# Performance work log

Measured on AMD Instinct MI355X. Metric: run time of the kernel, lower is better.

The kernel has to match this reference:

```python
import jax, jax.numpy as jnp
import numpy as np

B, S, D = 4, 2048, 1024
NEG_INF = jnp.float32(-jnp.inf)


def setup_inputs() -> dict:
    key = jax.random.key(0)
    kx, kq, kk, kv = jax.random.split(key, 4)
    scale = 0.02
    return {
        "x": jax.random.normal(kx, (B, S, D), dtype=jnp.float32),
        "Wq": jax.random.normal(kq, (D, D), dtype=jnp.float32) * scale,
        "Wk": jax.random.normal(kk, (D, D), dtype=jnp.float32) * scale,
        "Wv": jax.random.normal(kv, (D, D), dtype=jnp.float32) * scale,
    }


def reference(x, Wq, Wk, Wv):
    # nn.Linear(d_in, d_out): y = x @ W.T (no bias; qkv_bias=False)
    q = jnp.einsum("bsd,ed->bse", x, Wq)
    k = jnp.einsum("bsd,ed->bse", x, Wk)
    v = jnp.einsum("bsd,ed->bse", x, Wv)
    n = x.shape[1]
    scores = jnp.einsum("bqe,bke->bqk", q, k)  # [B, S, S]
    # causal mask: positions k > q are masked with -inf
    causal = jnp.tril(jnp.ones((n, n), dtype=bool))
    scores = jnp.where(causal[None, :, :], scores, NEG_INF)
    attn = jax.nn.softmax(scores / jnp.sqrt(jnp.float32(k.shape[-1])), axis=-1)
    # dropout p=0.0 (eval) -> identity
    return jnp.einsum("bqk,bke->bqe", attn, v)
```

## Files before the change

### kernel.cpp

```cpp
#include <hip/hip_runtime.h>
#include <hip/hip_bf16.h>
#include <stdint.h>
#include <stddef.h>


typedef __hip_bfloat16 bf16;
typedef short short8 __attribute__((ext_vector_type(8)));
typedef short short4v __attribute__((ext_vector_type(4)));
typedef float f32x4 __attribute__((ext_vector_type(4)));

#define BM 256
#define BN 128
#define BK 64
#define MSZ 8192
#define DD 1024

__device__ __forceinline__ void cstore(float* p, float v) { *p = v; }
__device__ __forceinline__ void cstore(bf16* p, float v) { *p = __float2bfloat16(v); }

__global__ __launch_bounds__(256)
void f2b(const float* __restrict__ s, bf16* __restrict__ d, int n) {
  const int i = (blockIdx.x * 256 + threadIdx.x) * 4;
  if (i >= n) return;
  const float4 v = *(const float4*)(s + i);
  bf16 t[4] = {__float2bfloat16(v.x), __float2bfloat16(v.y),
               __float2bfloat16(v.z), __float2bfloat16(v.w)};
  *(short4v*)(d + i) = *(short4v*)t;
}

__global__ __launch_bounds__(256)
void f2b3(const float* __restrict__ a, const float* __restrict__ b,
          const float* __restrict__ c, bf16* __restrict__ d, int n) {
  const float* s = (blockIdx.y == 0) ? a : (blockIdx.y == 1) ? b : c;
  const int i = (blockIdx.x * 256 + threadIdx.x) * 4;
  if (i >= n) return;
  const float4 v = *(const float4*)(s + i);
  bf16 t[4] = {__float2bfloat16(v.x), __float2bfloat16(v.y),
               __float2bfloat16(v.z), __float2bfloat16(v.w)};
  *(short4v*)(d + (size_t)blockIdx.y * n + i) = *(short4v*)t;
}

template <int MODE, typename CT>
__global__ __launch_bounds__(512, 4)
void gemm_bt(const bf16* __restrict__ A, const bf16* __restrict__ B,
             CT* __restrict__ C, bf16* __restrict__ C2,
             int lda, int ldb, int ldc, int K,
             long sA, long sB, long sC, float scale) {
  int by, bx;
  if (MODE == 2) {
    const int t = blockIdx.x;
    by = (int)((__fsqrt_rn(4.f * (float)t + 1.f) - 1.f) * 0.5f);
    while ((by + 1) * (by + 2) <= t) by++;
    while (by * (by + 1) > t) by--;
    bx = t - by * (by + 1);
  } else if (MODE == 3) {
    by = gridDim.y - 1 - blockIdx.y;
    bx = blockIdx.x;
  } else {
    by = blockIdx.y;
    bx = blockIdx.x;
  }

  __shared__ short8 As[2048];
  __shared__ short8 Bs[1024];

  const int tid = threadIdx.x;
  const int wave = tid >> 6, lane = tid & 63;
  const int wm = wave >> 1, wn = wave & 1;
  const int l15 = lane & 15, q4 = lane >> 4;
  const int bm0 = by * BM, bn0 = bx * BN;

  const bf16* Az = A + (long)blockIdx.z * sA;
  const bf16* Bz = B + (long)blockIdx.z * sB;
  CT* Cz = C + (long)blockIdx.z * sC;

  const int sg = lane >> 3, sr = lane & 7;
  const bf16* apg = Az + (size_t)(bm0 + wave * 32 + sr) * lda + sg * 8;
  const bf16* bpg = Bz + (size_t)(bn0 + wave * 16 + sr) * ldb + sg * 8;
  short8* asw = &As[wave * 256];
  short8* bsw = &Bs[wave * 128];

  const int Ke = (MODE == 3) ? min(K, (by + 1) * BM) : K;

  const int rh = l15 >> 3, r3 = l15 & 7;
  const int fra = wm * 512 + rh * 64 + q4 * 8 + r3;
  const int frb = wn * 512 + rh * 64 + q4 * 8 + r3;

  f32x4 acc[4][4] = {};

  for (int k0 = 0; k0 < Ke; k0 += BK) {
#pragma unroll
    for (int j = 0; j < 4; j++)
      __builtin_amdgcn_global_load_lds(apg + (size_t)j * 8 * lda + k0,
                                       asw + j * 64, 16, 0, 0);
#pragma unroll
    for (int j = 0; j < 2; j++)
      __builtin_amdgcn_global_load_lds(bpg + (size_t)j * 8 * ldb + k0,
                                       bsw + j * 64, 16, 0, 0);
    __syncthreads();

#pragma unroll
    for (int s = 0; s < 2; s++) {
      short8 af[4], bfr[4];
#pragma unroll
      for (int i = 0; i < 4; i++) af[i] = As[fra + i * 128 + s * 32];
#pragma unroll
      for (int j = 0; j < 4; j++) bfr[j] = Bs[frb + j * 128 + s * 32];
#pragma unroll
      for (int i = 0; i < 4; i++)
#pragma unroll
        for (int j = 0; j < 4; j++)
          acc[i][j] = __builtin_amdgcn_mfma_f32_16x16x32_bf16(af[i], bfr[j], acc[i][j], 0, 0, 0);
    }
    __syncthreads();
  }

  if (MODE == 1 && bx >= 16) {
#pragma unroll
    for (int i = 0; i < 4; i++) {
#pragma unroll
      for (int j = 0; j < 4; j++) {
        const int rowb = bm0 + wm * 64 + i * 16 + q4 * 4;
        const int v = (bn0 - 2048) + wn * 64 + j * 16 + l15;
        bf16 t[4] = {__float2bfloat16(acc[i][j][0]), __float2bfloat16(acc[i][j][1]),
                     __float2bfloat16(acc[i][j][2]), __float2bfloat16(acc[i][j][3])};
        *(short4v*)(C2 + (size_t)v * MSZ + rowb) = *(short4v*)t;
      }
    }
    return;
  }

  CT* Cb = Cz;
  int coff = bn0;
  if (MODE == 1) {
    Cb = Cz + (bx >= 8 ? (size_t)MSZ * DD : 0);
    coff = (bx & 7) * BN;
  }
#pragma unroll
  for (int i = 0; i < 4; i++) {
#pragma unroll
    for (int j = 0; j < 4; j++) {
#pragma unroll
      for (int r = 0; r < 4; r++) {
        const int row = bm0 + wm * 64 + i * 16 + q4 * 4 + r;
        const int col = coff + wn * 64 + j * 16 + l15;
        cstore(&Cb[(size_t)row * ldc + col], acc[i][j][r] * scale);
      }
    }
  }
}

__global__ __launch_bounds__(256)
void softmax_rows(const bf16* __restrict__ Sc, bf16* __restrict__ P, int S) {
  const int q = blockIdx.x, b = blockIdx.y;
  const short8* srow = (const short8*)(Sc + ((size_t)b * S + q) * S);
  short8* prow = (short8*)(P + ((size_t)b * S + q) * S);
  const int len = q + 1;
  const int tid = threadIdx.x;
  const int wave = tid >> 6, lane = tid & 63;
  __shared__ float red[10];

  const short8 raw = srow[tid];
  float v[8];
#pragma unroll
  for (int j = 0; j < 8; j++) {
    const int k = tid * 8 + j;
    const float f = __bfloat162float(((const bf16*)&raw)[j]);
    v[j] = (k < len) ? f : -1e30f;
  }

  float m = v[0];
#pragma unroll
  for (int j = 1; j < 8; j++) m = fmaxf(m, v[j]);
#pragma unroll
  for (int o = 32; o; o >>= 1) m = fmaxf(m, __shfl_down(m, o));
  if (lane == 0) red[wave] = m;
  __syncthreads();
  if (tid == 0) red[8] = fmaxf(fmaxf(red[0], red[1]), fmaxf(red[2], red[3]));
  __syncthreads();
  const float M = red[8];

  float e[8], s = 0.f;
#pragma unroll
  for (int j = 0; j < 8; j++) { e[j] = __expf(v[j] - M); s += e[j]; }
#pragma unroll
  for (int o = 32; o; o >>= 1) s += __shfl_down(s, o);
  if (lane == 0) red[4 + wave] = s;
  __syncthreads();
  if (tid == 0) red[9] = red[4] + red[5] + red[6] + red[7];
  __syncthreads();
  const float inv = 1.f / red[9];

  short8 outp;
#pragma unroll
  for (int j = 0; j < 8; j++) {
    const int k = tid * 8 + j;
    ((bf16*)&outp)[j] = __float2bfloat16((k < len) ? e[j] * inv : 0.f);
  }
  prow[tid] = outp;
}

extern "C" void kernel_launch(void* const* d_in, const int* in_sizes, int n_in,
                              void* d_out, int out_size, void* d_ws, size_t ws_size,
                              hipStream_t stream) {
  const float* x  = (const float*)d_in[0];
  const float* Wq = (const float*)d_in[1];
  const float* Wk = (const float*)d_in[2];
  const float* Wv = (const float*)d_in[3];
  float* out = (float*)d_out;

  const int Bb = 4, S = 2048, D = 1024, MS = Bb * S;

  char* ws = (char*)d_ws;
  bf16* xb = (bf16*)ws;
  bf16* wb = (bf16*)(ws + (size_t)MS * D * 2);
  bf16* Q  = (bf16*)(ws + (size_t)MS * D * 2 + 3u * D * D * 2);
  bf16* Kp = Q + (size_t)MS * D;
  bf16* VT = Kp + (size_t)MS * D;
  bf16* Sc = VT + (size_t)MS * D;
  bf16* P  = (bf16*)ws;
  (void)Kp;

  dim3 blk(256);
  dim3 blk5(512);

  f2b<<<dim3(MS * D / 4 / 256), blk, 0, stream>>>(x, xb, MS * D);
  f2b3<<<dim3(D * D / 4 / 256, 3), blk, 0, stream>>>(Wq, Wk, Wv, wb, D * D);

  gemm_bt<1, bf16><<<dim3(3 * D / BN, MS / BM, 1), blk5, 0, stream>>>(
      xb, wb, Q, VT, D, D, D, D, 0, 0, 0, 1.f);
  gemm_bt<2, bf16><<<dim3(72, 1, Bb), blk5, 0, stream>>>(
      Q, Kp, Sc, nullptr, D, D, S, D,
      (long)S * D, (long)S * D, (long)S * S, 0.03125f);
  softmax_rows<<<dim3(S, Bb), blk, 0, stream>>>(Sc, P, S);
  gemm_bt<3, float><<<dim3(D / BN, S / BM, Bb), blk5, 0, stream>>>(
      P, VT, out, nullptr, S, MS, D, S,
      (long)S * S, (long)S, (long)S * D, 1.f);
}
```

Measured before the change: 326.6 us.

## Pipeline GEMM with triple-buffered A and double-buffered B in LDS

Rewrites the bf16 GEMM main loop as a software pipeline. A is triple-buffered and B double-buffered in shared memory, async global-to-LDS loads are issued interleaved with MFMA phases, and waits use explicit vmcnt and barriers. It also remaps the 8 waves from a 4x2 to a 2x4 layout, with 128x32 per-wave tiles, and raises MFMA priority with setprio. The aim is to hide global load latency that the old load-sync-compute-sync loop exposed, at the cost of more LDS use (lower occupancy, launch bounds lowered to 2) and many barriers per iteration.

```diff
diff --git a/kernel.cpp b/kernel.cpp
--- a/kernel.cpp
+++ b/kernel.cpp
@@ -41,7 +41,7 @@
 }
 
 template <int MODE, typename CT>
-__global__ __launch_bounds__(512, 4)
+__global__ __launch_bounds__(512, 2)
 void gemm_bt(const bf16* __restrict__ A, const bf16* __restrict__ B,
              CT* __restrict__ C, bf16* __restrict__ C2,
              int lda, int ldb, int ldc, int K,
@@ -61,69 +61,132 @@
     bx = blockIdx.x;
   }
 
-  __shared__ short8 As[2048];
-  __shared__ short8 Bs[1024];
+  __shared__ short8 As[3 * 2048];
+  __shared__ short8 Bs[2 * 1024];
 
   const int tid = threadIdx.x;
   const int wave = tid >> 6, lane = tid & 63;
-  const int wm = wave >> 1, wn = wave & 1;
+  const int wm = wave >> 2, wn = wave & 3;
   const int l15 = lane & 15, q4 = lane >> 4;
+  const int rh = l15 >> 3, r3 = l15 & 7;
+  const int sg = lane >> 3, sr = lane & 7;
   const int bm0 = by * BM, bn0 = bx * BN;
 
   const bf16* Az = A + (long)blockIdx.z * sA;
   const bf16* Bz = B + (long)blockIdx.z * sB;
   CT* Cz = C + (long)blockIdx.z * sC;
 
-  const int sg = lane >> 3, sr = lane & 7;
-  const bf16* apg = Az + (size_t)(bm0 + wave * 32 + sr) * lda + sg * 8;
-  const bf16* bpg = Bz + (size_t)(bn0 + wave * 16 + sr) * ldb + sg * 8;
-  short8* asw = &As[wave * 256];
-  short8* bsw = &Bs[wave * 128];
+  const bf16* ap0 = Az + (size_t)(bm0 + wave * 16 + sr) * lda + sg * 8;
+  const bf16* bp0 = Bz + (size_t)(bn0 + wave * 16 + sr) * ldb + sg * 8;
 
   const int Ke = (MODE == 3) ? min(K, (by + 1) * BM) : K;
-
-  const int rh = l15 >> 3, r3 = l15 & 7;
-  const int fra = wm * 512 + rh * 64 + q4 * 8 + r3;
-  const int frb = wn * 512 + rh * 64 + q4 * 8 + r3;
-
-  f32x4 acc[4][4] = {};
-
-  for (int k0 = 0; k0 < Ke; k0 += BK) {
-#pragma unroll
-    for (int j = 0; j < 4; j++)
-      __builtin_amdgcn_global_load_lds(apg + (size_t)j * 8 * lda + k0,
-                                       asw + j * 64, 16, 0, 0);
+  const int NT = Ke >> 6;
+
+  auto stageA = [&](int slot, int half, int k0) {
+    short8* d = &As[slot * 2048 + half * 1024 + wave * 128];
+    const bf16* s = ap0 + (size_t)(half * 128) * lda + k0;
 #pragma unroll
     for (int j = 0; j < 2; j++)
-      __builtin_amdgcn_global_load_lds(bpg + (size_t)j * 8 * ldb + k0,
-                                       bsw + j * 64, 16, 0, 0);
-    __syncthreads();
-
-#pragma unroll
-    for (int s = 0; s < 2; s++) {
-      short8 af[4], bfr[4];
-#pragma unroll
-      for (int i = 0; i < 4; i++) af[i] = As[fra + i * 128 + s * 32];
-#pragma unroll
-      for (int j = 0; j < 4; j++) bfr[j] = Bs[frb + j * 128 + s * 32];
-#pragma unroll
-      for (int i = 0; i < 4; i++)
-#pragma unroll
-        for (int j = 0; j < 4; j++)
-          acc[i][j] = __builtin_amdgcn_mfma_f32_16x16x32_bf16(af[i], bfr[j], acc[i][j], 0, 0, 0);
-    }
-    __syncthreads();
+      __builtin_amdgcn_global_load_lds(s + (size_t)(j * 8) * lda, d + j * 64, 16, 0, 0);
+  };
+  auto stageB = [&](int slot, int k0) {
+    short8* d = &Bs[slot * 1024 + wave * 128];
+#pragma unroll
+    for (int j = 0; j < 2; j++)
+      __builtin_amdgcn_global_load_lds(bp0 + (size_t)(j * 8) * ldb + k0, d + j * 64, 16, 0, 0);
+  };
+
+  const int fa0 = wm * 1024 + rh * 64 + q4 * 8 + r3;
+  const int fb0 = wn * 256 + rh * 64 + q4 * 8 + r3;
+
+  f32x4 acc[8][2] = {};
+  short8 af[4], bf[2];
+
+  stageA(0, 0, 0);
+  stageA(0, 1, 0);
+  stageB(0, 0);
+  stageA(1, 0, 64);
+  stageA(1, 1, 64);
+  asm volatile("s_waitcnt vmcnt(4)" ::: "memory");
+  asm volatile("s_barrier" ::: "memory");
+
+  int sa = 0, sb = 0;
+  for (int t = 0; t < NT; ++t) {
+    const short8* Ac = &As[sa * 2048];
+    const short8* Bc = &Bs[sb * 1024];
+    const int sa2 = (sa >= 1) ? sa - 1 : 2;
+    const int kA = (t + 2) << 6, kB = (t + 1) << 6;
+
+#pragma unroll
+    for (int i = 0; i < 4; i++) af[i] = Ac[fa0 + i * 128];
+#pragma unroll
+    for (int j = 0; j < 2; j++) bf[j] = Bc[fb0 + j * 128];
+    if (t + 1 < NT) stageB(sb ^ 1, kB);
+    asm volatile("s_barrier" ::: "memory");
+    __builtin_amdgcn_s_setprio(1);
+#pragma unroll
+    for (int i = 0; i < 4; i++)
+#pragma unroll
+      for (int j = 0; j < 2; j++)
+        acc[i][j] = __builtin_amdgcn_mfma_f32_16x16x32_bf16(af[i], bf[j], acc[i][j], 0, 0, 0);
+    __builtin_amdgcn_s_setprio(0);
+    asm volatile("s_barrier" ::: "memory");
+
+#pragma unroll
+    for (int i = 0; i < 4; i++) af[i] = Ac[fa0 + 512 + i * 128];
+    if (t + 2 < NT) stageA(sa2, 0, kA);
+    asm volatile("s_barrier" ::: "memory");
+    __builtin_amdgcn_s_setprio(1);
+#pragma unroll
+    for (int i = 0; i < 4; i++)
+#pragma unroll
+      for (int j = 0; j < 2; j++)
+        acc[4 + i][j] = __builtin_amdgcn_mfma_f32_16x16x32_bf16(af[i], bf[j], acc[4 + i][j], 0, 0, 0);
+    __builtin_amdgcn_s_setprio(0);
+    asm volatile("s_barrier" ::: "memory");
+
+#pragma unroll
+    for (int i = 0; i < 4; i++) af[i] = Ac[fa0 + 32 + i * 128];
+#pragma unroll
+    for (int j = 0; j < 2; j++) bf[j] = Bc[fb0 + 32 + j * 128];
+    if (t + 2 < NT) stageA(sa2, 1, kA);
+    asm volatile("s_barrier" ::: "memory");
+    __builtin_amdgcn_s_setprio(1);
+#pragma unroll
+    for (int i = 0; i < 4; i++)
+#pragma unroll
+      for (int j = 0; j < 2; j++)
+        acc[i][j] = __builtin_amdgcn_mfma_f32_16x16x32_bf16(af[i], bf[j], acc[i][j], 0, 0, 0);
+    __builtin_amdgcn_s_setprio(0);
+    asm volatile("s_barrier" ::: "memory");
+
+#pragma unroll
+    for (int i = 0; i < 4; i++) af[i] = Ac[fa0 + 512 + 32 + i * 128];
+    if (t + 2 < NT) asm volatile("s_waitcnt vmcnt(4)" ::: "memory");
+    else            asm volatile("s_waitcnt vmcnt(0)" ::: "memory");
+    asm volatile("s_barrier" ::: "memory");
+    __builtin_amdgcn_s_setprio(1);
+#pragma unroll
+    for (int i = 0; i < 4; i++)
+#pragma unroll
+      for (int j = 0; j < 2; j++)
+        acc[4 + i][j] = __builtin_amdgcn_mfma_f32_16x16x32_bf16(af[i], bf[j], acc[4 + i][j], 0, 0, 0);
+    __builtin_amdgcn_s_setprio(0);
+    asm volatile("s_barrier" ::: "memory");
+
+    sa = (sa == 2) ? 0 : sa + 1;
+    sb ^= 1;
   }
 
   if (MODE == 1 && bx >= 16) {
 #pragma unroll
-    for (int i = 0; i < 4; i++) {
-#pragma unroll
-      for (int j = 0; j < 4; j++) {
-        const int rowb = bm0 + wm * 64 + i * 16 + q4 * 4;
-        const int v = (bn0 - 2048) + wn * 64 + j * 16 + l15;
-        bf16 t[4] = {__float2bfloat16(acc[i][j][0]), __float2bfloat16(acc[i][j][1]),
-                     __float2bfloat16(acc[i][j][2]), __float2bfloat16(acc[i][j][3])};
+    for (int I = 0; I < 8; I++) {
+#pragma unroll
+      for (int j = 0; j < 2; j++) {
+        const int rowb = bm0 + wm * 128 + I * 16 + q4 * 4;
+        const int v = (bn0 - 2048) + wn * 32 + j * 16 + l15;
+        bf16 t[4] = {__float2bfloat16(acc[I][j][0]), __float2bfloat16(acc[I][j][1]),
+                     __float2bfloat16(acc[I][j][2]), __float2bfloat16(acc[I][j][3])};
         *(short4v*)(C2 + (size_t)v * MSZ + rowb) = *(short4v*)t;
       }
     }
@@ -137,14 +200,14 @@
     coff = (bx & 7) * BN;
   }
 #pragma unroll
-  for (int i = 0; i < 4; i++) {
-#pragma unroll
-    for (int j = 0; j < 4; j++) {
+  for (int I = 0; I < 8; I++) {
+#pragma unroll
+    for (int j = 0; j < 2; j++) {
 #pragma unroll
       for (int r = 0; r < 4; r++) {
-        const int row = bm0 + wm * 64 + i * 16 + q4 * 4 + r;
-        const int col = coff + wn * 64 + j * 16 + l15;
-        cstore(&Cb[(size_t)row * ldc + col], acc[i][j][r] * scale);
+        const int row = bm0 + wm * 128 + I * 16 + q4 * 4 + r;
+        const int col = coff + wn * 32 + j * 16 + l15;
+        cstore(&Cb[(size_t)row * ldc + col], acc[I][j][r] * scale);
       }
     }
   }
```

Result: slower. 343.2 us (+5.1%).
